# Optimization experiments

Hardware: AMD Instinct MI355X
Metric: run time of the kernel (lower is better)

## Reference

```python
import math
import jax, jax.numpy as jnp
import numpy as np

B, S, D = 4, 2048, 1024
H, HD = 16, 64
NUM_BUCKETS = 32
MAX_DISTANCE = 128
EPS = 1e-6
ENC_S = 512


def _relative_position_bucket(relative_position):
    # bidirectional=False path
    num_buckets = NUM_BUCKETS
    rp = -jnp.minimum(relative_position, 0)  # [S, S] nonneg
    max_exact = num_buckets // 2
    is_small = rp < max_exact
    scale = (num_buckets - max_exact) / math.log(MAX_DISTANCE / max_exact)
    large = max_exact + (jnp.log(jnp.maximum(rp, 1).astype(jnp.float32) / max_exact) * scale).astype(jnp.int32)
    large = jnp.minimum(large, num_buckets - 1)
    return jnp.where(is_small, rp, large)


def compute_bias(rel_emb, q_len, k_len):
    ctx = jnp.arange(q_len)[:, None]
    mem = jnp.arange(k_len)[None, :]
    bucket = _relative_position_bucket(mem - ctx)          # [q, k] int
    values = rel_emb[bucket]                                # [q, k, H]
    return jnp.transpose(values, (2, 0, 1))[None]           # [1, H, q, k]


def setup_inputs() -> dict:
    key = jax.random.key(0)
    ks = jax.random.split(key, 8)
    std = 0.02
    return {
        "input_ids": jax.random.normal(ks[0], (B, S, D), jnp.float32),
        "encoder_output": jax.random.normal(ks[1], (B, ENC_S, D), jnp.float32),
        "wq": jax.random.normal(ks[2], (D, H * HD), jnp.float32) * std,
        "wk": jax.random.normal(ks[3], (D, H * HD), jnp.float32) * std,
        "wv": jax.random.normal(ks[4], (D, H * HD), jnp.float32) * std,
        "wo": jax.random.normal(ks[5], (H * HD, D), jnp.float32) * std,
        "rel_emb": jax.random.normal(ks[6], (NUM_BUCKETS, H), jnp.float32) * std,
        "ln_w": jnp.ones((D,), jnp.float32),
    }


def reference(input_ids, encoder_output, wq, wk, wv, wo, rel_emb, ln_w):
    origin = input_ids
    # MT5LayerNorm: RMS norm, no mean subtraction, no bias
    variance = jnp.mean(jnp.square(input_ids.astype(jnp.float32)), axis=-1, keepdims=True)
    x = (input_ids * jax.lax.rsqrt(variance + EPS)) * ln_w

    q = (x @ wq).reshape(B, S, H, HD)
    k = (x @ wk).reshape(B, S, H, HD)
    v = (x @ wv).reshape(B, S, H, HD)

    # NOTE: T5-style attention has no 1/sqrt(d) scaling
    scores = jnp.einsum("bqhd,bkhd->bhqk", q, k)
    scores = scores + compute_bias(rel_emb, S, S)
    attn = jax.nn.softmax(scores, axis=-1)
    ctx = jnp.einsum("bhqk,bkhd->bqhd", attn, v).reshape(B, S, H * HD)
    attn_out = ctx @ wo

    # residual connection (dropout is identity at rate 0 / eval)
    return origin + attn_out
```

## Files before the change

kernel.cpp:

```cpp
#include <hip/hip_runtime.h>
#include <hip/hip_bf16.h>
#include <math.h>

#define S_LEN 2048
#define D_DIM 1024
#define NHEAD 16

typedef __attribute__((ext_vector_type(8))) short bf16x8;
typedef __attribute__((ext_vector_type(4))) float floatx4;

__device__ __forceinline__ short f32_bf16(float f) {
  union { float f; unsigned u; } v; v.f = f;
  unsigned r = v.u + 0x7FFFu + ((v.u >> 16) & 1u);
  return (short)(r >> 16);
}

__device__ __forceinline__ float exp2_fast(float x) {
#if __has_builtin(__builtin_amdgcn_exp2f)
  return __builtin_amdgcn_exp2f(x);
#else
  float r; asm("v_exp_f32 %0, %1" : "=v"(r) : "v"(x)); return r;
#endif
}

__device__ __forceinline__ void gload16(const void* g, void* l) {
  __builtin_amdgcn_global_load_lds((const __attribute__((address_space(1))) unsigned*)g,
                                   (__attribute__((address_space(3))) unsigned*)l,
                                   16, 0, 0);
}

__global__ __launch_bounds__(256) void rmsnorm_k(const float* __restrict__ x,
                                                 const float* __restrict__ w,
                                                 short* __restrict__ out) {
  int row = blockIdx.x;
  const float4* xr = (const float4*)(x + (size_t)row * D_DIM);
  float4 v = xr[threadIdx.x];
  float ss = v.x*v.x + v.y*v.y + v.z*v.z + v.w*v.w;
  #pragma unroll
  for (int off = 32; off > 0; off >>= 1) ss += __shfl_xor(ss, off);
  __shared__ float red[4];
  if ((threadIdx.x & 63) == 0) red[threadIdx.x >> 6] = ss;
  __syncthreads();
  float scale = rsqrtf((red[0]+red[1]+red[2]+red[3]) * (1.f/D_DIM) + 1e-6f);
  float4 wv = ((const float4*)w)[threadIdx.x];
  short4 o;
  o.x = f32_bf16(v.x*scale*wv.x);
  o.y = f32_bf16(v.y*scale*wv.y);
  o.z = f32_bf16(v.z*scale*wv.z);
  o.w = f32_bf16(v.w*scale*wv.w);
  ((short4*)out)[(size_t)row*256 + threadIdx.x] = o;
}

__global__ __launch_bounds__(256) void pack_wqkv_k(const float* __restrict__ wq,
                                                   const float* __restrict__ wk,
                                                   const float* __restrict__ wv,
                                                   short* __restrict__ o) {
  int t = blockIdx.x*256 + threadIdx.x;
  int n = t >> 10, k = t & 1023;
  const float* src = (n < 1024) ? wq : ((n < 2048) ? wk : wv);
  float scale = (n < 1024) ? 1.44269504f : 1.0f;
  o[t] = f32_bf16(src[(size_t)k*1024 + (n & 1023)] * scale);
}

__global__ __launch_bounds__(256) void pack_wo_k(const float* __restrict__ wo,
                                                 short* __restrict__ o) {
  int t = blockIdx.x*256 + threadIdx.x;
  int n = t >> 10, k = t & 1023;
  o[t] = f32_bf16(wo[(size_t)k*1024 + n]);
}

template<bool ADD_RES>
__global__ __launch_bounds__(256) void gemm_bt(const short* __restrict__ A,
                                               const short* __restrict__ Bt,
                                               short* __restrict__ Cb,
                                               float* __restrict__ Cf,
                                               const float* __restrict__ res,
                                               int M, int N, int K) {
  constexpr int BK = 32;
  __shared__ __align__(16) short As[128*BK];
  __shared__ __align__(16) short Bs[128*BK];
  int tid = threadIdx.x;
  int w = tid >> 6, lane = tid & 63, quad = lane >> 4, l16 = lane & 15;
  int wr = w >> 1, wc = w & 1;
  int bn = blockIdx.x, bm = blockIdx.y;
  const short* Ag = A + (size_t)bm * 128 * K;
  const short* Bg = Bt + (size_t)bn * 128 * K;
  int r4 = lane >> 2, c4 = lane & 3;

  floatx4 acc[4][4] = {};

  for (int k0 = 0; k0 < K; k0 += BK) {
    #pragma unroll
    for (int i = 0; i < 2; i++) {
      int c = w + i*4;
      gload16(Ag + (size_t)(c*16 + r4) * K + k0 + c4*8, &As[c*16*BK]);
      gload16(Bg + (size_t)(c*16 + r4) * K + k0 + c4*8, &Bs[c*16*BK]);
    }
    __syncthreads();
    bf16x8 af[4], bfr[4];
    #pragma unroll
    for (int i = 0; i < 4; i++) {
      af[i]  = *(const bf16x8*)&As[(wr*64 + i*16 + l16)*BK + quad*8];
      bfr[i] = *(const bf16x8*)&Bs[(wc*64 + i*16 + l16)*BK + quad*8];
    }
    #pragma unroll
    for (int i = 0; i < 4; i++)
      #pragma unroll
      for (int j = 0; j < 4; j++)
        acc[i][j] = __builtin_amdgcn_mfma_f32_16x16x32_bf16(af[i], bfr[j], acc[i][j], 0, 0, 0);
    __syncthreads();
  }

  #pragma unroll
  for (int i = 0; i < 4; i++) {
    int row0 = bm*128 + wr*64 + i*16 + quad*4;
    #pragma unroll
    for (int j = 0; j < 4; j++) {
      int col = bn*128 + wc*64 + j*16 + l16;
      #pragma unroll
      for (int r = 0; r < 4; r++) {
        size_t idx = (size_t)(row0 + r) * N + col;
        if (ADD_RES) Cf[idx] = res[idx] + acc[i][j][r];
        else         Cb[idx] = f32_bf16(acc[i][j][r]);
      }
    }
  }
}

__global__ __launch_bounds__(256) void pack_vt_k(const short* __restrict__ qkv,
                                                 short* __restrict__ vt) {
  __shared__ __align__(16) short tile[64][72];
  int s0 = blockIdx.x * 64;
  int bh = blockIdx.y;
  int b = bh >> 4, h = bh & 15;
  int t = threadIdx.x;
  #pragma unroll
  for (int i = 0; i < 2; i++) {
    int idx = t + i*256;
    int s = idx >> 3, c = idx & 7;
    *(bf16x8*)&tile[s][c*8] =
      *(const bf16x8*)&qkv[(size_t)(b*S_LEN + s0 + s)*3072 + 2048 + h*64 + c*8];
  }
  __syncthreads();
  #pragma unroll
  for (int i = 0; i < 2; i++) {
    int idx = t + i*256;
    int hd = idx >> 3, c = idx & 7;
    short tmp[8];
    #pragma unroll
    for (int j = 0; j < 8; j++) tmp[j] = tile[c*8 + j][hd];
    *(bf16x8*)&vt[((size_t)(bh*64 + hd))*S_LEN + s0 + c*8] = *(bf16x8*)tmp;
  }
}

__global__ __launch_bounds__(256) void flash_k(const short* __restrict__ qkv,
                                               const short* __restrict__ vt,
                                               const float* __restrict__ rel_emb,
                                               short* __restrict__ ctx) {
  __shared__ __align__(16) short Kb[2][64*64];
  __shared__ __align__(16) short Vb[2][64*64];
  __shared__ float lut2[132];

  const int qt = blockIdx.x, bh = blockIdx.y;
  const int b = bh >> 4, h = bh & 15;
  const int t = threadIdx.x, w = t >> 6, lane = t & 63, quad = lane >> 4, l16 = lane & 15;
  const float L2E = 1.44269504f;

  if (t < 129) {
    int rp = t, bucket;
    if (rp < 16) bucket = rp;
    else {
      bucket = 16 + (int)(logf((float)rp * 0.0625f) * (16.f / logf(8.f)));
      if (bucket > 31) bucket = 31;
    }
    lut2[t] = rel_emb[bucket*16 + h] * L2E;
  }
  const float bfut  = rel_emb[h] * L2E;
  const float bpast = rel_emb[31*16 + h] * L2E;
  const floatx4 bf4 = {bfut, bfut, bfut, bfut};
  const floatx4 bp4 = {bpast, bpast, bpast, bpast};
  const floatx4 zz4 = {0.f, 0.f, 0.f, 0.f};

  const int srow = lane >> 3;
  const int slc  = (lane & 7) ^ srow;
  const int kperm = 32*(w >> 1) + 8*(srow >> 2) + 4*(w & 1) + (srow & 3);

  bf16x8 qB[2][2];
  #pragma unroll
  for (int rb = 0; rb < 2; rb++) {
    const short* qb = qkv + ((size_t)(b*S_LEN + qt*128 + rb*64 + w*16 + l16))*3072 + h*64;
    qB[rb][0] = *(const bf16x8*)&qb[quad*8];
    qB[rb][1] = *(const bf16x8*)&qb[32 + quad*8];
  }

  floatx4 o[2][4] = {};
  floatx4 li4[2] = {};
  const short ONE = (short)0x3F80;
  bf16x8 onesA = {ONE, ONE, ONE, ONE, ONE, ONE, ONE, ONE};

  const int swz0 = (quad     ^ (l16 & 7)) * 8;
  const int swz1 = ((quad+4) ^ (l16 & 7)) * 8;

  #define STAGE(p_, kt_) do {                                                   \
    const short* kg_ = qkv + ((size_t)(b*S_LEN + (kt_)*64 + kperm))*3072 + 1024 + h*64 + slc*8; \
    gload16(kg_,            &Kb[p_][(w*16    )*64]);                            \
    gload16(kg_ + 16*3072,  &Kb[p_][(w*16 + 8)*64]);                            \
    const short* vg_ = vt + ((size_t)(bh*64 + w*16 + srow))*2048 + (kt_)*64 + slc*8; \
    gload16(vg_,            &Vb[p_][(w*16    )*64]);                            \
    gload16(vg_ + 8*2048,   &Vb[p_][(w*16 + 8)*64]);                            \
  } while (0)

  STAGE(0, 0);
  int p = 0;

  for (int kt = 0; kt < 32; kt++) {
    __syncthreads();

    bool boundary = (kt >= 2*qt - 2) && (kt <= 2*qt + 1);
    floatx4 cinit = boundary ? zz4 : ((kt >= 2*qt) ? bf4 : bp4);

    floatx4 sc[2][4];
    #pragma unroll
    for (int c = 0; c < 4; c++) {
      int rowA = (c*16 + l16)*64;
      bf16x8 ka0 = *(const bf16x8*)&Kb[p][rowA + swz0];
      bf16x8 ka1 = *(const bf16x8*)&Kb[p][rowA + swz1];
      #pragma unroll
      for (int rb = 0; rb < 2; rb++) {
        floatx4 z = __builtin_amdgcn_mfma_f32_16x16x32_bf16(ka0, qB[rb][0], cinit, 0, 0, 0);
        z = __builtin_amdgcn_mfma_f32_16x16x32_bf16(ka1, qB[rb][1], z, 0, 0, 0);
        sc[rb][c] = z;
      }
    }

    if (boundary) {
      #pragma unroll
      for (int rb = 0; rb < 2; rb++) {
        int q0 = qt*128 + rb*64 + w*16 + l16;
        #pragma unroll
        for (int c = 0; c < 4; c++) {
          int kk = kt*64 + 32*(c >> 1) + 8*quad + 4*(c & 1);
          #pragma unroll
          for (int r = 0; r < 4; r++) {
            int d = q0 - (kk + r);
            d = d < 0 ? 0 : (d > 128 ? 128 : d);
            sc[rb][c][r] += lut2[d];
          }
        }
      }
    }

    #pragma unroll
    for (int rb = 0; rb < 2; rb++)
      #pragma unroll
      for (int c = 0; c < 4; c++)
        #pragma unroll
        for (int r = 0; r < 4; r++)
          sc[rb][c][r] = exp2_fast(sc[rb][c][r]);

    if (kt < 31) STAGE(p^1, kt+1);

    bf16x8 pf[2][2];
    #pragma unroll
    for (int rb = 0; rb < 2; rb++) {
      #pragma unroll
      for (int hh = 0; hh < 2; hh++) {
        union { bf16x8 v; unsigned u[4]; } pk;
        floatx4 a = sc[rb][2*hh], bb = sc[rb][2*hh + 1];
        pk.u[0] = __builtin_amdgcn_perm(__float_as_uint(a[1]),  __float_as_uint(a[0]),  0x07060302);
        pk.u[1] = __builtin_amdgcn_perm(__float_as_uint(a[3]),  __float_as_uint(a[2]),  0x07060302);
        pk.u[2] = __builtin_amdgcn_perm(__float_as_uint(bb[1]), __float_as_uint(bb[0]), 0x07060302);
        pk.u[3] = __builtin_amdgcn_perm(__float_as_uint(bb[3]), __float_as_uint(bb[2]), 0x07060302);
        pf[rb][hh] = pk.v;
      }
    }

    #pragma unroll
    for (int rb = 0; rb < 2; rb++) {
      li4[rb] = __builtin_amdgcn_mfma_f32_16x16x32_bf16(onesA, pf[rb][0], li4[rb], 0, 0, 0);
      li4[rb] = __builtin_amdgcn_mfma_f32_16x16x32_bf16(onesA, pf[rb][1], li4[rb], 0, 0, 0);
    }
    #pragma unroll
    for (int jj = 0; jj < 4; jj++) {
      int rowV = (jj*16 + l16)*64;
      bf16x8 va0 = *(const bf16x8*)&Vb[p][rowV + swz0];
      bf16x8 va1 = *(const bf16x8*)&Vb[p][rowV + swz1];
      #pragma unroll
      for (int rb = 0; rb < 2; rb++) {
        o[rb][jj] = __builtin_amdgcn_mfma_f32_16x16x32_bf16(va0, pf[rb][0], o[rb][jj], 0, 0, 0);
        o[rb][jj] = __builtin_amdgcn_mfma_f32_16x16x32_bf16(va1, pf[rb][1], o[rb][jj], 0, 0, 0);
      }
    }
    p ^= 1;
  }

  #pragma unroll
  for (int rb = 0; rb < 2; rb++) {
    float inv = 1.f / li4[rb][0];
    size_t row = (size_t)(b*S_LEN + qt*128 + rb*64 + w*16 + l16);
    #pragma unroll
    for (int jj = 0; jj < 4; jj++) {
      short4 st;
      st.x = f32_bf16(o[rb][jj][0] * inv);
      st.y = f32_bf16(o[rb][jj][1] * inv);
      st.z = f32_bf16(o[rb][jj][2] * inv);
      st.w = f32_bf16(o[rb][jj][3] * inv);
      *(short4*)&ctx[row*1024 + h*64 + jj*16 + quad*4] = st;
    }
  }
  #undef STAGE
}

extern "C" void kernel_launch(void* const* d_in, const int* in_sizes, int n_in,
                              void* d_out, int out_size, void* d_ws, size_t ws_size,
                              hipStream_t stream) {
  const float* input_ids = (const float*)d_in[0];
  const float* wq      = (const float*)d_in[2];
  const float* wk      = (const float*)d_in[3];
  const float* wv      = (const float*)d_in[4];
  const float* wo      = (const float*)d_in[5];
  const float* rel_emb = (const float*)d_in[6];
  const float* ln_w    = (const float*)d_in[7];
  float* out = (float*)d_out;

  char* ws = (char*)d_ws;
  short* xb     = (short*)ws;  ws += (size_t)8192*1024*2;
  short* wqkv_t = (short*)ws;  ws += (size_t)3072*1024*2;
  short* wo_t   = (short*)ws;  ws += (size_t)1024*1024*2;
  short* qkv    = (short*)ws;  ws += (size_t)8192*3072*2;
  short* vt     = (short*)ws;  ws += (size_t)64*64*2048*2;
  short* ctx    = (short*)ws;  ws += (size_t)8192*1024*2;

  rmsnorm_k<<<8192, 256, 0, stream>>>(input_ids, ln_w, xb);
  pack_wqkv_k<<<(3072*1024)/256, 256, 0, stream>>>(wq, wk, wv, wqkv_t);
  pack_wo_k<<<(1024*1024)/256, 256, 0, stream>>>(wo, wo_t);
  gemm_bt<false><<<dim3(24, 64), 256, 0, stream>>>(xb, wqkv_t, qkv, nullptr, nullptr,
                                                   8192, 3072, 1024);
  pack_vt_k<<<dim3(32, 64), 256, 0, stream>>>(qkv, vt);
  flash_k<<<dim3(16, 64), 256, 0, stream>>>(qkv, vt, rel_emb, ctx);
  gemm_bt<true><<<dim3(8, 64), 256, 0, stream>>>(ctx, wo_t, nullptr, out, input_ids,
                                                 8192, 1024, 1024);
}
```

Baseline: 328.2 us.

## Double GEMM K-tile with XOR-swizzled LDS and unroll attention loop by two

The GEMM's K tile grows from 32 to 64, halving the number of barrier pairs per output tile. Its shared-memory layout gains an XOR swizzle so the wider rows can be read without bank conflicts. The attention inner loop is manually unrolled by two with constant buffer indices and precomputed base pointers, so the ping-pong index becomes compile-time and per-iteration address arithmetic shrinks. The cost is doubled GEMM LDS (32 KB per block), which may lower occupancy, and larger code size in the attention kernel.

```diff
diff --git a/kernel.cpp b/kernel.cpp
--- a/kernel.cpp
+++ b/kernel.cpp
@@ -76,7 +76,7 @@
                                                float* __restrict__ Cf,
                                                const float* __restrict__ res,
                                                int M, int N, int K) {
-  constexpr int BK = 32;
+  constexpr int BK = 64;
   __shared__ __align__(16) short As[128*BK];
   __shared__ __align__(16) short Bs[128*BK];
   int tid = threadIdx.x;
@@ -85,29 +85,34 @@
   int bn = blockIdx.x, bm = blockIdx.y;
   const short* Ag = A + (size_t)bm * 128 * K;
   const short* Bg = Bt + (size_t)bn * 128 * K;
-  int r4 = lane >> 2, c4 = lane & 3;
+  const int srow = lane >> 3;
+  const int slc  = (lane & 7) ^ srow;
 
   floatx4 acc[4][4] = {};
 
   for (int k0 = 0; k0 < K; k0 += BK) {
     #pragma unroll
-    for (int i = 0; i < 2; i++) {
-      int c = w + i*4;
-      gload16(Ag + (size_t)(c*16 + r4) * K + k0 + c4*8, &As[c*16*BK]);
-      gload16(Bg + (size_t)(c*16 + r4) * K + k0 + c4*8, &Bs[c*16*BK]);
+    for (int i = 0; i < 4; i++) {
+      int rbase = w*32 + i*8;
+      gload16(Ag + (size_t)(rbase + srow) * K + k0 + slc*8, &As[rbase*BK]);
+      gload16(Bg + (size_t)(rbase + srow) * K + k0 + slc*8, &Bs[rbase*BK]);
     }
     __syncthreads();
-    bf16x8 af[4], bfr[4];
-    #pragma unroll
-    for (int i = 0; i < 4; i++) {
-      af[i]  = *(const bf16x8*)&As[(wr*64 + i*16 + l16)*BK + quad*8];
-      bfr[i] = *(const bf16x8*)&Bs[(wc*64 + i*16 + l16)*BK + quad*8];
-    }
-    #pragma unroll
-    for (int i = 0; i < 4; i++)
+    #pragma unroll
+    for (int h = 0; h < 2; h++) {
+      int sw = ((quad + 4*h) ^ (l16 & 7)) * 8;
+      bf16x8 af[4], bfr[4];
       #pragma unroll
-      for (int j = 0; j < 4; j++)
-        acc[i][j] = __builtin_amdgcn_mfma_f32_16x16x32_bf16(af[i], bfr[j], acc[i][j], 0, 0, 0);
+      for (int i = 0; i < 4; i++) {
+        af[i]  = *(const bf16x8*)&As[(wr*64 + i*16 + l16)*BK + sw];
+        bfr[i] = *(const bf16x8*)&Bs[(wc*64 + i*16 + l16)*BK + sw];
+      }
+      #pragma unroll
+      for (int i = 0; i < 4; i++)
+        #pragma unroll
+        for (int j = 0; j < 4; j++)
+          acc[i][j] = __builtin_amdgcn_mfma_f32_16x16x32_bf16(af[i], bfr[j], acc[i][j], 0, 0, 0);
+    }
     __syncthreads();
   }
 
@@ -185,6 +190,11 @@
   const int slc  = (lane & 7) ^ srow;
   const int kperm = 32*(w >> 1) + 8*(srow >> 2) + 4*(w & 1) + (srow & 3);
 
+  const short* kgU = qkv + ((size_t)b*S_LEN)*3072 + 1024 + h*64;
+  const int    loK = kperm*3072 + slc*8;
+  const short* vgU = vt + ((size_t)bh*64)*2048;
+  const int    loV = (w*16 + srow)*2048 + slc*8;
+
   bf16x8 qB[2][2];
   #pragma unroll
   for (int rb = 0; rb < 2; rb++) {
@@ -201,97 +211,92 @@
   const int swz0 = (quad     ^ (l16 & 7)) * 8;
   const int swz1 = ((quad+4) ^ (l16 & 7)) * 8;
 
-  #define STAGE(p_, kt_) do {                                                   \
-    const short* kg_ = qkv + ((size_t)(b*S_LEN + (kt_)*64 + kperm))*3072 + 1024 + h*64 + slc*8; \
-    gload16(kg_,            &Kb[p_][(w*16    )*64]);                            \
-    gload16(kg_ + 16*3072,  &Kb[p_][(w*16 + 8)*64]);                            \
-    const short* vg_ = vt + ((size_t)(bh*64 + w*16 + srow))*2048 + (kt_)*64 + slc*8; \
-    gload16(vg_,            &Vb[p_][(w*16    )*64]);                            \
-    gload16(vg_ + 8*2048,   &Vb[p_][(w*16 + 8)*64]);                            \
+  #define STAGE(P_, KT_) do {                                                   \
+    const short* ka_ = kgU + (size_t)(KT_)*196608 + loK;                        \
+    gload16(ka_,          &Kb[P_][(w*16    )*64]);                              \
+    gload16(ka_ + 49152,  &Kb[P_][(w*16 + 8)*64]);                              \
+    const short* va_ = vgU + loV + (KT_)*64;                                    \
+    gload16(va_,          &Vb[P_][(w*16    )*64]);                              \
+    gload16(va_ + 16384,  &Vb[P_][(w*16 + 8)*64]);                              \
   } while (0)
 
+  #define BODY(P_, KT_) do {                                                    \
+    __syncthreads();                                                            \
+    bool boundary = ((KT_) >= 2*qt - 2) && ((KT_) <= 2*qt + 1);                 \
+    floatx4 cinit = boundary ? zz4 : (((KT_) >= 2*qt) ? bf4 : bp4);             \
+    floatx4 sc[2][4];                                                           \
+    _Pragma("unroll")                                                           \
+    for (int c = 0; c < 4; c++) {                                               \
+      int rowA = (c*16 + l16)*64;                                               \
+      bf16x8 ka0 = *(const bf16x8*)&Kb[P_][rowA + swz0];                        \
+      bf16x8 ka1 = *(const bf16x8*)&Kb[P_][rowA + swz1];                        \
+      _Pragma("unroll")                                                         \
+      for (int rb = 0; rb < 2; rb++) {                                          \
+        floatx4 z = __builtin_amdgcn_mfma_f32_16x16x32_bf16(ka0, qB[rb][0], cinit, 0, 0, 0); \
+        z = __builtin_amdgcn_mfma_f32_16x16x32_bf16(ka1, qB[rb][1], z, 0, 0, 0);\
+        sc[rb][c] = z;                                                          \
+      }                                                                         \
+    }                                                                           \
+    if (boundary) {                                                             \
+      _Pragma("unroll")                                                         \
+      for (int rb = 0; rb < 2; rb++) {                                          \
+        int q0 = qt*128 + rb*64 + w*16 + l16;                                   \
+        _Pragma("unroll")                                                       \
+        for (int c = 0; c < 4; c++) {                                           \
+          int kk = (KT_)*64 + 32*(c >> 1) + 8*quad + 4*(c & 1);                 \
+          _Pragma("unroll")                                                     \
+          for (int r = 0; r < 4; r++) {                                         \
+            int d = q0 - (kk + r);                                              \
+            d = d < 0 ? 0 : (d > 128 ? 128 : d);                                \
+            sc[rb][c][r] += lut2[d];                                            \
+          }                                                                     \
+        }                                                                       \
+      }                                                                         \
+    }                                                                           \
+    _Pragma("unroll")                                                           \
+    for (int rb = 0; rb < 2; rb++)                                              \
+      _Pragma("unroll")                                                         \
+      for (int c = 0; c < 4; c++)                                               \
+        _Pragma("unroll")                                                       \
+        for (int r = 0; r < 4; r++)                                             \
+          sc[rb][c][r] = exp2_fast(sc[rb][c][r]);                               \
+    if ((KT_) < 31) STAGE((P_) ^ 1, (KT_) + 1);                                 \
+    bf16x8 pf[2][2];                                                            \
+    _Pragma("unroll")                                                           \
+    for (int rb = 0; rb < 2; rb++) {                                            \
+      _Pragma("unroll")                                                         \
+      for (int hh = 0; hh < 2; hh++) {                                          \
+        union { bf16x8 v; unsigned u[4]; } pk;                                  \
+        floatx4 a = sc[rb][2*hh], bb = sc[rb][2*hh + 1];                        \
+        pk.u[0] = __builtin_amdgcn_perm(__float_as_uint(a[1]),  __float_as_uint(a[0]),  0x07060302); \
+        pk.u[1] = __builtin_amdgcn_perm(__float_as_uint(a[3]),  __float_as_uint(a[2]),  0x07060302); \
+        pk.u[2] = __builtin_amdgcn_perm(__float_as_uint(bb[1]), __float_as_uint(bb[0]), 0x07060302); \
+        pk.u[3] = __builtin_amdgcn_perm(__float_as_uint(bb[3]), __float_as_uint(bb[2]), 0x07060302); \
+        pf[rb][hh] = pk.v;                                                      \
+      }                                                                         \
+    }                                                                           \
+    _Pragma("unroll")                                                           \
+    for (int rb = 0; rb < 2; rb++) {                                            \
+      li4[rb] = __builtin_amdgcn_mfma_f32_16x16x32_bf16(onesA, pf[rb][0], li4[rb], 0, 0, 0); \
+      li4[rb] = __builtin_amdgcn_mfma_f32_16x16x32_bf16(onesA, pf[rb][1], li4[rb], 0, 0, 0); \
+    }                                                                           \
+    _Pragma("unroll")                                                           \
+    for (int jj = 0; jj < 4; jj++) {                                            \
+      int rowV = (jj*16 + l16)*64;                                              \
+      bf16x8 va0 = *(const bf16x8*)&Vb[P_][rowV + swz0];                        \
+      bf16x8 va1 = *(const bf16x8*)&Vb[P_][rowV + swz1];                        \
+      _Pragma("unroll")                                                         \
+      for (int rb = 0; rb < 2; rb++) {                                          \
+        o[rb][jj] = __builtin_amdgcn_mfma_f32_16x16x32_bf16(va0, pf[rb][0], o[rb][jj], 0, 0, 0); \
+        o[rb][jj] = __builtin_amdgcn_mfma_f32_16x16x32_bf16(va1, pf[rb][1], o[rb][jj], 0, 0, 0); \
+      }                                                                         \
+    }                                                                           \
+  } while (0)
+
   STAGE(0, 0);
-  int p = 0;
-
-  for (int kt = 0; kt < 32; kt++) {
-    __syncthreads();
-
-    bool boundary = (kt >= 2*qt - 2) && (kt <= 2*qt + 1);
-    floatx4 cinit = boundary ? zz4 : ((kt >= 2*qt) ? bf4 : bp4);
-
-    floatx4 sc[2][4];
-    #pragma unroll
-    for (int c = 0; c < 4; c++) {
-      int rowA = (c*16 + l16)*64;
-      bf16x8 ka0 = *(const bf16x8*)&Kb[p][rowA + swz0];
-      bf16x8 ka1 = *(const bf16x8*)&Kb[p][rowA + swz1];
-      #pragma unroll
-      for (int rb = 0; rb < 2; rb++) {
-        floatx4 z = __builtin_amdgcn_mfma_f32_16x16x32_bf16(ka0, qB[rb][0], cinit, 0, 0, 0);
-        z = __builtin_amdgcn_mfma_f32_16x16x32_bf16(ka1, qB[rb][1], z, 0, 0, 0);
-        sc[rb][c] = z;
-      }
-    }
-
-    if (boundary) {
-      #pragma unroll
-      for (int rb = 0; rb < 2; rb++) {
-        int q0 = qt*128 + rb*64 + w*16 + l16;
-        #pragma unroll
-        for (int c = 0; c < 4; c++) {
-          int kk = kt*64 + 32*(c >> 1) + 8*quad + 4*(c & 1);
-          #pragma unroll
-          for (int r = 0; r < 4; r++) {
-            int d = q0 - (kk + r);
-            d = d < 0 ? 0 : (d > 128 ? 128 : d);
-            sc[rb][c][r] += lut2[d];
-          }
-        }
-      }
-    }
-
-    #pragma unroll
-    for (int rb = 0; rb < 2; rb++)
-      #pragma unroll
-      for (int c = 0; c < 4; c++)
-        #pragma unroll
-        for (int r = 0; r < 4; r++)
-          sc[rb][c][r] = exp2_fast(sc[rb][c][r]);
-
-    if (kt < 31) STAGE(p^1, kt+1);
-
-    bf16x8 pf[2][2];
-    #pragma unroll
-    for (int rb = 0; rb < 2; rb++) {
-      #pragma unroll
-      for (int hh = 0; hh < 2; hh++) {
-        union { bf16x8 v; unsigned u[4]; } pk;
-        floatx4 a = sc[rb][2*hh], bb = sc[rb][2*hh + 1];
-        pk.u[0] = __builtin_amdgcn_perm(__float_as_uint(a[1]),  __float_as_uint(a[0]),  0x07060302);
-        pk.u[1] = __builtin_amdgcn_perm(__float_as_uint(a[3]),  __float_as_uint(a[2]),  0x07060302);
-        pk.u[2] = __builtin_amdgcn_perm(__float_as_uint(bb[1]), __float_as_uint(bb[0]), 0x07060302);
-        pk.u[3] = __builtin_amdgcn_perm(__float_as_uint(bb[3]), __float_as_uint(bb[2]), 0x07060302);
-        pf[rb][hh] = pk.v;
-      }
-    }
-
-    #pragma unroll
-    for (int rb = 0; rb < 2; rb++) {
-      li4[rb] = __builtin_amdgcn_mfma_f32_16x16x32_bf16(onesA, pf[rb][0], li4[rb], 0, 0, 0);
-      li4[rb] = __builtin_amdgcn_mfma_f32_16x16x32_bf16(onesA, pf[rb][1], li4[rb], 0, 0, 0);
-    }
-    #pragma unroll
-    for (int jj = 0; jj < 4; jj++) {
-      int rowV = (jj*16 + l16)*64;
-      bf16x8 va0 = *(const bf16x8*)&Vb[p][rowV + swz0];
-      bf16x8 va1 = *(const bf16x8*)&Vb[p][rowV + swz1];
-      #pragma unroll
-      for (int rb = 0; rb < 2; rb++) {
-        o[rb][jj] = __builtin_amdgcn_mfma_f32_16x16x32_bf16(va0, pf[rb][0], o[rb][jj], 0, 0, 0);
-        o[rb][jj] = __builtin_amdgcn_mfma_f32_16x16x32_bf16(va1, pf[rb][1], o[rb][jj], 0, 0, 0);
-      }
-    }
-    p ^= 1;
+  for (int kt = 0; kt < 32; kt += 2) {
+    BODY(0, kt);
+    BODY(1, kt + 1);
   }
 
   #pragma unroll
@@ -309,6 +314,7 @@
     }
   }
   #undef STAGE
+  #undef BODY
 }
 
 extern "C" void kernel_launch(void* const* d_in, const int* in_sizes, int n_in,
```

New measurement: 321.8 us. No clear change (-2.0%).
